# Kernel optimization log

Hardware: AMD Instinct MI355X
Metric: run time of the kernel (lower is better)

The kernel has to match this reference:

```python
import jax, jax.numpy as jnp
import numpy as np

FREQ_NUM = 3
MAX_STEP = 4
PERIODS = np.array([24.0, 7.0, 365.0], dtype=np.float32)  # ceil(sups - infs)
INFS = np.array([0.0, 0.0, 0.0], dtype=np.float32)
BS, H, W, L, D = 128, 56, 56, 64, 128
Z_DIM = 3 * H * W + L * D + D            # 17728
EMB_DIM = 2 * FREQ_NUM                   # sin/cos per frequency
IN_DIM = Z_DIM + 2 * EMB_DIM             # 17740
HID = 4096
N_POI, N_USER = 5000, 1000


def setup_inputs() -> dict:
    key = jax.random.key(0)
    ks = jax.random.split(key, 10)
    sups = jnp.asarray(PERIODS)
    return {
        "input_freq": jax.random.uniform(ks[0], (BS, H, W), jnp.float32),
        "input_seq": jax.random.randint(ks[1], (BS, L), 0, N_POI),
        "uid": jax.random.randint(ks[2], (BS,), 0, N_USER),
        "cur_time": jax.random.uniform(ks[3], (BS, FREQ_NUM), jnp.float32) * sups,
        "tar_time": jax.random.uniform(ks[4], (BS, FREQ_NUM), jnp.float32) * sups,
        "fuse_embed": jax.random.normal(ks[5], (N_POI + N_USER, D), jnp.float32),
        "W1": jax.random.normal(ks[6], (IN_DIM, HID), jnp.float32) / np.sqrt(IN_DIM),
        "b1": jnp.zeros((HID,), jnp.float32),
        "W2": jax.random.normal(ks[7], (HID, Z_DIM), jnp.float32) / np.sqrt(HID),
        "b2": jnp.zeros((Z_DIM,), jnp.float32),
        "n_poi": N_POI,
    }


def _time_grid(cur_time, tar_time):
    # Per-sample linspace with periodic wraparound; snapshot t0_ after each
    # micro-step assignment (intended semantics of the torch loop).
    periods = jnp.asarray(PERIODS)
    frac = jnp.linspace(0.0, 1.0, MAX_STEP)  # [4]
    rows = []
    t_cur = cur_time
    for j in range(FREQ_NUM):
        s = cur_time[:, j]
        e = tar_time[:, j]
        wrap = s > e
        e_adj = jnp.where(wrap, e + periods[j], e)
        inter = s[:, None] + (e_adj - s)[:, None] * frac[None, :]  # [bs,4]
        inter = jnp.where(wrap[:, None], jnp.mod(inter, periods[j]), inter)
        for k in range(MAX_STEP):
            t_cur = t_cur.at[:, j].set(inter[:, k])
            rows.append(t_cur)
    return jnp.stack(rows, axis=0)  # [4*freq_num, bs, freq_num]


def _time_embedding(T):
    # sinusoidal embedding per frequency band
    phase = 2.0 * jnp.pi * (T - jnp.asarray(INFS)) / jnp.asarray(PERIODS)
    return jnp.concatenate([jnp.sin(phase), jnp.cos(phase)], axis=-1)  # [S,bs,2F]


def reference(input_freq, input_seq, uid, cur_time, tar_time, fuse_embed,
              W1, b1, W2, b2, n_poi):
    bs = input_freq.shape[0]
    A = jnp.tile(input_freq[:, None], (1, 3, 1, 1)).reshape(bs, -1)     # [bs,3HW]
    x = fuse_embed[input_seq].transpose(0, 2, 1).reshape(bs, -1)        # [bs,D*L]
    u = fuse_embed[n_poi + uid].reshape(bs, -1)                          # [bs,D]
    z0 = jnp.concatenate([A, x, u], axis=-1)                             # [bs,Z_DIM]

    T = _time_grid(cur_time, tar_time)
    emb = _time_embedding(T)                                             # [S,bs,2F]

    def step(z, te):
        t0e, t1e = te
        inp = jnp.concatenate([z, t0e, t1e], axis=-1)
        dz = jnp.tanh(inp @ W1 + b1) @ W2 + b2
        return z + dz, None

    z, _ = jax.lax.scan(step, z0, (emb[:-1], emb[1:]))
    return z
```

## Files before the change

kernel.cpp:

```cpp
#include <hip/hip_runtime.h>
#include <math.h>

typedef __bf16 bf16;
typedef __bf16 bf16x8 __attribute__((ext_vector_type(8)));
typedef float f32x4 __attribute__((ext_vector_type(4)));

#define ZDIM 17728
#define HIDN 4096
#define BSZ 128
#define KC1 24
#define KC2 4

__device__ __forceinline__ void gl_lds16(const bf16* g, bf16* l) {
  __builtin_amdgcn_global_load_lds(
      (const __attribute__((address_space(1))) unsigned int*)g,
      (__attribute__((address_space(3))) unsigned int*)l, 16, 0, 0);
}

__global__ void k_cast_transpose(const float* __restrict__ src, bf16* __restrict__ dst,
                                 int K, int N) {
  __shared__ float t[64][33];
  int tx = threadIdx.x, ty = threadIdx.y;
  int n0 = blockIdx.x * 32, k0 = blockIdx.y * 64;
#pragma unroll
  for (int i = 0; i < 64; i += 8)
    t[ty + i][tx] = src[(size_t)(k0 + ty + i) * N + (n0 + tx)];
  __syncthreads();
#pragma unroll
  for (int i = 0; i < 32; i += 8) {
    int nl = ty + i;
    union { bf16 h[2]; unsigned u; } p;
    p.h[0] = (bf16)t[2 * tx][nl];
    p.h[1] = (bf16)t[2 * tx + 1][nl];
    *(unsigned*)&dst[(size_t)(n0 + nl) * K + k0 + 2 * tx] = p.u;
  }
}

__global__ void k_build_z0(const float* __restrict__ input_freq, const int* __restrict__ seq,
                           const int* __restrict__ uid, const float* __restrict__ fuse,
                           const int* __restrict__ n_poi_p,
                           float* __restrict__ z, bf16* __restrict__ zb) {
  int n = blockIdx.x * 256 + threadIdx.x;
  int b = blockIdx.y;
  if (n >= ZDIM) return;
  float v;
  if (n < 9408) {
    v = input_freq[b * 3136 + (n % 3136)];
  } else if (n < 17600) {
    int m = n - 9408;
    int d = m >> 6, l = m & 63;
    v = fuse[(size_t)seq[b * 64 + l] * 128 + d];
  } else {
    int d = n - 17600;
    v = fuse[(size_t)(n_poi_p[0] + uid[b]) * 128 + d];
  }
  size_t idx = (size_t)b * ZDIM + n;
  z[idx] = v;
  zb[idx] = (bf16)v;
}

__global__ void k_build_emb(const float* __restrict__ cur, const float* __restrict__ tar,
                            float* __restrict__ E) {
  int b = threadIdx.x;
  const float P[3] = {24.0f, 7.0f, 365.0f};
  const float TWO_PI = 6.283185307179586f;
  float t[3];
  for (int c = 0; c < 3; ++c) t[c] = cur[b * 3 + c];
  int r = 0;
  for (int j = 0; j < 3; ++j) {
    float s = cur[b * 3 + j], e = tar[b * 3 + j];
    bool wrap = s > e;
    float ea = wrap ? (e + P[j]) : e;
    for (int k = 0; k < 4; ++k) {
      float frac = (float)k / 3.0f;
      float v = s + (ea - s) * frac;
      if (wrap) v = v - floorf(v / P[j]) * P[j];
      t[j] = v;
      for (int c = 0; c < 3; ++c) {
        float ph = TWO_PI * t[c] / P[c];
        E[(r * BSZ + b) * 6 + c] = sinf(ph);
        E[(r * BSZ + b) * 6 + 3 + c] = cosf(ph);
      }
      ++r;
    }
  }
}

__global__ __launch_bounds__(256, 3) void k_gemm1(const bf16* __restrict__ A,
                                                  const bf16* __restrict__ Bt,
                                                  float* __restrict__ P) {
  __shared__ __align__(16) bf16 As[128 * 32];
  __shared__ __align__(16) bf16 Bs[128 * 32];
  const int tid = threadIdx.x;
  const int w = tid >> 6, lane = tid & 63;
  const int q = lane >> 4, r = lane & 15;
  const int nt = blockIdx.x, kc = blockIdx.y;
  const int nsteps = 23 + (kc < 2 ? 1 : 0);
  const int kstart = kc * 23 + (kc < 2 ? kc : 2);

  const int srow = lane >> 2, sslot = lane & 3;
  const int sg = sslot ^ ((srow >> 2) & 3);
  const int rA0 = (2 * w) * 16 + srow;
  const int rA1 = (2 * w + 1) * 16 + srow;
  long k0 = (long)kstart * 32;
  const bf16* pA0 = A + (size_t)rA0 * ZDIM + k0 + sg * 8;
  const bf16* pA1 = A + (size_t)rA1 * ZDIM + k0 + sg * 8;
  const bf16* pB0 = Bt + (size_t)(nt * 128 + rA0) * ZDIM + k0 + sg * 8;
  const bf16* pB1 = Bt + (size_t)(nt * 128 + rA1) * ZDIM + k0 + sg * 8;
  bf16* lA0 = &As[(2 * w) * 512];
  bf16* lA1 = &As[(2 * w + 1) * 512];
  bf16* lB0 = &Bs[(2 * w) * 512];
  bf16* lB1 = &Bs[(2 * w + 1) * 512];

  const int swr = (r >> 2) & 3;
  const int aoff = r * 32 + (q ^ swr) * 8;
  const int boff0 = (32 * w + r) * 32 + (q ^ swr) * 8;
  const int boff1 = boff0 + 512;

  f32x4 zero4 = {0.f, 0.f, 0.f, 0.f};
  f32x4 acc[8][2];
#pragma unroll
  for (int mb = 0; mb < 8; ++mb) { acc[mb][0] = zero4; acc[mb][1] = zero4; }

  for (int s = 0; s < nsteps; ++s) {
    gl_lds16(pA0, lA0); gl_lds16(pA1, lA1);
    gl_lds16(pB0, lB0); gl_lds16(pB1, lB1);
    pA0 += 32; pA1 += 32; pB0 += 32; pB1 += 32;
    __syncthreads();
    bf16x8 bfr0 = *(const bf16x8*)&Bs[boff0];
    bf16x8 bfr1 = *(const bf16x8*)&Bs[boff1];
#pragma unroll
    for (int mb = 0; mb < 8; ++mb) {
      bf16x8 afr = *(const bf16x8*)&As[mb * 512 + aoff];
      acc[mb][0] = __builtin_amdgcn_mfma_f32_16x16x32_bf16(afr, bfr0, acc[mb][0], 0, 0, 0);
      acc[mb][1] = __builtin_amdgcn_mfma_f32_16x16x32_bf16(afr, bfr1, acc[mb][1], 0, 0, 0);
    }
    __syncthreads();
  }

  float* Pk = P + (size_t)kc * (BSZ * HIDN);
#pragma unroll
  for (int i = 0; i < 2; ++i) {
    int n = nt * 128 + (2 * w + i) * 16 + r;
#pragma unroll
    for (int mb = 0; mb < 8; ++mb) {
#pragma unroll
      for (int reg = 0; reg < 4; ++reg) {
        int brow = mb * 16 + q * 4 + reg;
        Pk[(size_t)brow * HIDN + n] = acc[mb][i][reg];
      }
    }
  }
}

__global__ void k_epi1(const float* __restrict__ P, const float* __restrict__ b1,
                       const float* __restrict__ W1, const float* __restrict__ E,
                       int step, bf16* __restrict__ Hb) {
  int idx = blockIdx.x * 256 + threadIdx.x;
  int b = idx >> 12, n = idx & 4095;
  float s = b1[n];
#pragma unroll
  for (int c = 0; c < KC1; ++c) s += P[((size_t)c * BSZ + b) * HIDN + n];
  const float* e0 = E + ((size_t)step * BSZ + b) * 6;
  const float* e1 = e0 + BSZ * 6;
#pragma unroll
  for (int j = 0; j < 6; ++j) {
    s += e0[j] * W1[(size_t)(ZDIM + j) * HIDN + n];
    s += e1[j] * W1[(size_t)(ZDIM + 6 + j) * HIDN + n];
  }
  Hb[idx] = (bf16)tanhf(s);
}

__global__ __launch_bounds__(256, 4) void k_gemm2(const bf16* __restrict__ A,
                                                  const bf16* __restrict__ Bt,
                                                  float* __restrict__ P2) {
  __shared__ __align__(16) bf16 As[128 * 32];
  __shared__ __align__(16) bf16 Bs[64 * 32];
  const int tid = threadIdx.x;
  const int w = tid >> 6, lane = tid & 63;
  const int q = lane >> 4, r = lane & 15;
  const int nt = blockIdx.x;
  const int kc = blockIdx.y;
  const long k0 = (long)kc * 32 * 32;

  const int srow = lane >> 2, sslot = lane & 3;
  const int sg = sslot ^ ((srow >> 2) & 3);
  const int rA0 = (2 * w) * 16 + srow;
  const int rA1 = (2 * w + 1) * 16 + srow;
  const int rB = w * 16 + srow;
  const bf16* pA0 = A + (size_t)rA0 * HIDN + k0 + sg * 8;
  const bf16* pA1 = A + (size_t)rA1 * HIDN + k0 + sg * 8;
  const bf16* pB = Bt + (size_t)(nt * 64 + rB) * HIDN + k0 + sg * 8;
  bf16* lA0 = &As[(2 * w) * 512];
  bf16* lA1 = &As[(2 * w + 1) * 512];
  bf16* lB = &Bs[w * 512];

  const int swr = (r >> 2) & 3;
  const int aoff = r * 32 + (q ^ swr) * 8;
  const int boff = (w * 16 + r) * 32 + (q ^ swr) * 8;

  f32x4 zero4 = {0.f, 0.f, 0.f, 0.f};
  f32x4 acc[8];
#pragma unroll
  for (int mb = 0; mb < 8; ++mb) acc[mb] = zero4;

  for (int s = 0; s < 32; ++s) {
    gl_lds16(pA0, lA0); gl_lds16(pA1, lA1); gl_lds16(pB, lB);
    pA0 += 32; pA1 += 32; pB += 32;
    __syncthreads();
    bf16x8 bfr = *(const bf16x8*)&Bs[boff];
#pragma unroll
    for (int mb = 0; mb < 8; ++mb) {
      bf16x8 afr = *(const bf16x8*)&As[mb * 512 + aoff];
      acc[mb] = __builtin_amdgcn_mfma_f32_16x16x32_bf16(afr, bfr, acc[mb], 0, 0, 0);
    }
    __syncthreads();
  }

  float* Pk = P2 + (size_t)kc * (BSZ * ZDIM);
  int n = nt * 64 + w * 16 + r;
#pragma unroll
  for (int mb = 0; mb < 8; ++mb) {
#pragma unroll
    for (int reg = 0; reg < 4; ++reg) {
      int brow = mb * 16 + q * 4 + reg;
      Pk[(size_t)brow * ZDIM + n] = acc[mb][reg];
    }
  }
}

__global__ void k_epi2(const float* __restrict__ P2, const float* __restrict__ b2,
                       float* __restrict__ z, bf16* __restrict__ zb) {
  int idx = blockIdx.x * 256 + threadIdx.x;
  int n = idx % ZDIM;
  float s = b2[n];
#pragma unroll
  for (int c = 0; c < KC2; ++c) s += P2[(size_t)c * (BSZ * ZDIM) + idx];
  float v = z[idx] + s;
  z[idx] = v;
  zb[idx] = (bf16)v;
}

extern "C" void kernel_launch(void* const* d_in, const int* in_sizes, int n_in,
                              void* d_out, int out_size, void* d_ws, size_t ws_size,
                              hipStream_t stream) {
  const float* input_freq = (const float*)d_in[0];
  const int* seq = (const int*)d_in[1];
  const int* uid = (const int*)d_in[2];
  const float* cur = (const float*)d_in[3];
  const float* tar = (const float*)d_in[4];
  const float* fuse = (const float*)d_in[5];
  const float* W1 = (const float*)d_in[6];
  const float* b1 = (const float*)d_in[7];
  const float* W2 = (const float*)d_in[8];
  const float* b2 = (const float*)d_in[9];
  const int* n_poi = (const int*)d_in[10];
  float* z = (float*)d_out;

  char* ws = (char*)d_ws;
  bf16* W1t = (bf16*)ws;
  bf16* W2t = (bf16*)(ws + 145227776);
  bf16* Zb = (bf16*)(ws + 290455552);
  bf16* Hb = (bf16*)(ws + 294993920);
  float* P = (float*)(ws + 296042496);
  float* P2 = (float*)(ws + 296042496 + 50331648);
  float* E = (float*)(ws + 296042496 + 50331648 + 36306944);

  k_cast_transpose<<<dim3(HIDN / 32, ZDIM / 64), dim3(32, 8), 0, stream>>>(W1, W1t, ZDIM, HIDN);
  k_cast_transpose<<<dim3(ZDIM / 32, HIDN / 64), dim3(32, 8), 0, stream>>>(W2, W2t, HIDN, ZDIM);
  k_build_z0<<<dim3(70, BSZ), 256, 0, stream>>>(input_freq, seq, uid, fuse, n_poi, z, Zb);
  k_build_emb<<<1, BSZ, 0, stream>>>(cur, tar, E);

  for (int s = 0; s < 11; ++s) {
    k_gemm1<<<dim3(32, KC1), 256, 0, stream>>>(Zb, W1t, P);
    k_epi1<<<2048, 256, 0, stream>>>(P, b1, W1, E, s, Hb);
    k_gemm2<<<dim3(277, KC2), 256, 0, stream>>>(Hb, W2t, P2);
    k_epi2<<<8864, 256, 0, stream>>>(P2, b2, z, Zb);
  }
}
```

Measured before the change: 2.141 ms.

## Replace LDS-staged GEMMs with unified register-direct MFMA kernel and coalesce z0 gather

```diff
diff --git a/kernel.cpp b/kernel.cpp
--- a/kernel.cpp
+++ b/kernel.cpp
@@ -8,14 +8,8 @@
 #define ZDIM 17728
 #define HIDN 4096
 #define BSZ 128
-#define KC1 24
+#define KC1 16
 #define KC2 4
-
-__device__ __forceinline__ void gl_lds16(const bf16* g, bf16* l) {
-  __builtin_amdgcn_global_load_lds(
-      (const __attribute__((address_space(1))) unsigned int*)g,
-      (__attribute__((address_space(3))) unsigned int*)l, 16, 0, 0);
-}
 
 __global__ void k_cast_transpose(const float* __restrict__ src, bf16* __restrict__ dst,
                                  int K, int N) {
@@ -40,23 +34,32 @@
                            const int* __restrict__ uid, const float* __restrict__ fuse,
                            const int* __restrict__ n_poi_p,
                            float* __restrict__ z, bf16* __restrict__ zb) {
-  int n = blockIdx.x * 256 + threadIdx.x;
-  int b = blockIdx.y;
-  if (n >= ZDIM) return;
-  float v;
-  if (n < 9408) {
-    v = input_freq[b * 3136 + (n % 3136)];
-  } else if (n < 17600) {
-    int m = n - 9408;
+  __shared__ float X[64 * 129];
+  int b = blockIdx.x, tid = threadIdx.x;
+  float* zr = z + (size_t)b * ZDIM;
+  bf16* zbr = zb + (size_t)b * ZDIM;
+  for (int n = tid; n < 9408; n += 256) {
+    float v = input_freq[b * 3136 + (n % 3136)];
+    zr[n] = v; zbr[n] = (bf16)v;
+  }
+  {
+    int l = tid >> 2, c0 = (tid & 3) * 32;
+    const float* srcr = fuse + (size_t)seq[b * 64 + l] * 128 + c0;
+    float* dstr = X + l * 129 + c0;
+#pragma unroll
+    for (int i = 0; i < 32; i += 4)
+      *(f32x4*)&dstr[i] = *(const f32x4*)&srcr[i];
+  }
+  __syncthreads();
+  for (int m = tid; m < 8192; m += 256) {
     int d = m >> 6, l = m & 63;
-    v = fuse[(size_t)seq[b * 64 + l] * 128 + d];
-  } else {
-    int d = n - 17600;
-    v = fuse[(size_t)(n_poi_p[0] + uid[b]) * 128 + d];
-  }
-  size_t idx = (size_t)b * ZDIM + n;
-  z[idx] = v;
-  zb[idx] = (bf16)v;
+    float v = X[l * 129 + d];
+    zr[9408 + m] = v; zbr[9408 + m] = (bf16)v;
+  }
+  if (tid < 128) {
+    float v = fuse[(size_t)(n_poi_p[0] + uid[b]) * 128 + tid];
+    zr[17600 + tid] = v; zbr[17600 + tid] = (bf16)v;
+  }
 }
 
 __global__ void k_build_emb(const float* __restrict__ cur, const float* __restrict__ tar,
@@ -86,69 +89,47 @@
   }
 }
 
-__global__ __launch_bounds__(256, 3) void k_gemm1(const bf16* __restrict__ A,
-                                                  const bf16* __restrict__ Bt,
-                                                  float* __restrict__ P) {
-  __shared__ __align__(16) bf16 As[128 * 32];
-  __shared__ __align__(16) bf16 Bs[128 * 32];
+__global__ __launch_bounds__(256, 4) void k_gemm_rr(const bf16* __restrict__ A,
+                                                    const bf16* __restrict__ Bt,
+                                                    float* __restrict__ P,
+                                                    int Kdim, int Nout,
+                                                    int base, int rem) {
   const int tid = threadIdx.x;
   const int w = tid >> 6, lane = tid & 63;
   const int q = lane >> 4, r = lane & 15;
   const int nt = blockIdx.x, kc = blockIdx.y;
-  const int nsteps = 23 + (kc < 2 ? 1 : 0);
-  const int kstart = kc * 23 + (kc < 2 ? kc : 2);
-
-  const int srow = lane >> 2, sslot = lane & 3;
-  const int sg = sslot ^ ((srow >> 2) & 3);
-  const int rA0 = (2 * w) * 16 + srow;
-  const int rA1 = (2 * w + 1) * 16 + srow;
-  long k0 = (long)kstart * 32;
-  const bf16* pA0 = A + (size_t)rA0 * ZDIM + k0 + sg * 8;
-  const bf16* pA1 = A + (size_t)rA1 * ZDIM + k0 + sg * 8;
-  const bf16* pB0 = Bt + (size_t)(nt * 128 + rA0) * ZDIM + k0 + sg * 8;
-  const bf16* pB1 = Bt + (size_t)(nt * 128 + rA1) * ZDIM + k0 + sg * 8;
-  bf16* lA0 = &As[(2 * w) * 512];
-  bf16* lA1 = &As[(2 * w + 1) * 512];
-  bf16* lB0 = &Bs[(2 * w) * 512];
-  bf16* lB1 = &Bs[(2 * w + 1) * 512];
-
-  const int swr = (r >> 2) & 3;
-  const int aoff = r * 32 + (q ^ swr) * 8;
-  const int boff0 = (32 * w + r) * 32 + (q ^ swr) * 8;
-  const int boff1 = boff0 + 512;
-
-  f32x4 zero4 = {0.f, 0.f, 0.f, 0.f};
-  f32x4 acc[8][2];
-#pragma unroll
-  for (int mb = 0; mb < 8; ++mb) { acc[mb][0] = zero4; acc[mb][1] = zero4; }
-
+  const int nsteps = base + (kc < rem ? 1 : 0);
+  const long kstart = ((long)kc * base + (kc < rem ? kc : rem)) * 32;
+
+  const int n0 = nt * 64 + w * 16 + r;
+  const bf16* pB = Bt + (size_t)n0 * Kdim + kstart + q * 8;
+  const bf16* pA[8];
+#pragma unroll
+  for (int mb = 0; mb < 8; ++mb)
+    pA[mb] = A + (size_t)(mb * 16 + r) * Kdim + kstart + q * 8;
+
+  f32x4 acc[8] = {};
+#pragma unroll 2
   for (int s = 0; s < nsteps; ++s) {
-    gl_lds16(pA0, lA0); gl_lds16(pA1, lA1);
-    gl_lds16(pB0, lB0); gl_lds16(pB1, lB1);
-    pA0 += 32; pA1 += 32; pB0 += 32; pB1 += 32;
-    __syncthreads();
-    bf16x8 bfr0 = *(const bf16x8*)&Bs[boff0];
-    bf16x8 bfr1 = *(const bf16x8*)&Bs[boff1];
-#pragma unroll
-    for (int mb = 0; mb < 8; ++mb) {
-      bf16x8 afr = *(const bf16x8*)&As[mb * 512 + aoff];
-      acc[mb][0] = __builtin_amdgcn_mfma_f32_16x16x32_bf16(afr, bfr0, acc[mb][0], 0, 0, 0);
-      acc[mb][1] = __builtin_amdgcn_mfma_f32_16x16x32_bf16(afr, bfr1, acc[mb][1], 0, 0, 0);
-    }
-    __syncthreads();
-  }
-
-  float* Pk = P + (size_t)kc * (BSZ * HIDN);
-#pragma unroll
-  for (int i = 0; i < 2; ++i) {
-    int n = nt * 128 + (2 * w + i) * 16 + r;
-#pragma unroll
-    for (int mb = 0; mb < 8; ++mb) {
-#pragma unroll
-      for (int reg = 0; reg < 4; ++reg) {
-        int brow = mb * 16 + q * 4 + reg;
-        Pk[(size_t)brow * HIDN + n] = acc[mb][i][reg];
-      }
+    bf16x8 bfr = *(const bf16x8*)pB;
+    bf16x8 af[8];
+#pragma unroll
+    for (int mb = 0; mb < 8; ++mb) af[mb] = *(const bf16x8*)pA[mb];
+#pragma unroll
+    for (int mb = 0; mb < 8; ++mb)
+      acc[mb] = __builtin_amdgcn_mfma_f32_16x16x32_bf16(af[mb], bfr, acc[mb], 0, 0, 0);
+    pB += 32;
+#pragma unroll
+    for (int mb = 0; mb < 8; ++mb) pA[mb] += 32;
+  }
+
+  float* Pk = P + (size_t)kc * (BSZ * (size_t)Nout);
+#pragma unroll
+  for (int mb = 0; mb < 8; ++mb) {
+#pragma unroll
+    for (int reg = 0; reg < 4; ++reg) {
+      int m = mb * 16 + q * 4 + reg;
+      Pk[(size_t)m * Nout + n0] = acc[mb][reg];
     }
   }
 }
@@ -169,64 +150,6 @@
     s += e1[j] * W1[(size_t)(ZDIM + 6 + j) * HIDN + n];
   }
   Hb[idx] = (bf16)tanhf(s);
-}
-
-__global__ __launch_bounds__(256, 4) void k_gemm2(const bf16* __restrict__ A,
-                                                  const bf16* __restrict__ Bt,
-                                                  float* __restrict__ P2) {
-  __shared__ __align__(16) bf16 As[128 * 32];
-  __shared__ __align__(16) bf16 Bs[64 * 32];
-  const int tid = threadIdx.x;
-  const int w = tid >> 6, lane = tid & 63;
-  const int q = lane >> 4, r = lane & 15;
-  const int nt = blockIdx.x;
-  const int kc = blockIdx.y;
-  const long k0 = (long)kc * 32 * 32;
-
-  const int srow = lane >> 2, sslot = lane & 3;
-  const int sg = sslot ^ ((srow >> 2) & 3);
-  const int rA0 = (2 * w) * 16 + srow;
-  const int rA1 = (2 * w + 1) * 16 + srow;
-  const int rB = w * 16 + srow;
-  const bf16* pA0 = A + (size_t)rA0 * HIDN + k0 + sg * 8;
-  const bf16* pA1 = A + (size_t)rA1 * HIDN + k0 + sg * 8;
-  const bf16* pB = Bt + (size_t)(nt * 64 + rB) * HIDN + k0 + sg * 8;
-  bf16* lA0 = &As[(2 * w) * 512];
-  bf16* lA1 = &As[(2 * w + 1) * 512];
-  bf16* lB = &Bs[w * 512];
-
-  const int swr = (r >> 2) & 3;
-  const int aoff = r * 32 + (q ^ swr) * 8;
-  const int boff = (w * 16 + r) * 32 + (q ^ swr) * 8;
-
-  f32x4 zero4 = {0.f, 0.f, 0.f, 0.f};
-  f32x4 acc[8];
-#pragma unroll
-  for (int mb = 0; mb < 8; ++mb) acc[mb] = zero4;
-
-  for (int s = 0; s < 32; ++s) {
-    gl_lds16(pA0, lA0); gl_lds16(pA1, lA1); gl_lds16(pB, lB);
-    pA0 += 32; pA1 += 32; pB += 32;
-    __syncthreads();
-    bf16x8 bfr = *(const bf16x8*)&Bs[boff];
-#pragma unroll
-    for (int mb = 0; mb < 8; ++mb) {
-      bf16x8 afr = *(const bf16x8*)&As[mb * 512 + aoff];
-      acc[mb] = __builtin_amdgcn_mfma_f32_16x16x32_bf16(afr, bfr, acc[mb], 0, 0, 0);
-    }
-    __syncthreads();
-  }
-
-  float* Pk = P2 + (size_t)kc * (BSZ * ZDIM);
-  int n = nt * 64 + w * 16 + r;
-#pragma unroll
-  for (int mb = 0; mb < 8; ++mb) {
-#pragma unroll
-    for (int reg = 0; reg < 4; ++reg) {
-      int brow = mb * 16 + q * 4 + reg;
-      Pk[(size_t)brow * ZDIM + n] = acc[mb][reg];
-    }
-  }
 }
 
 __global__ void k_epi2(const float* __restrict__ P2, const float* __restrict__ b2,
@@ -263,18 +186,18 @@
   bf16* Zb = (bf16*)(ws + 290455552);
   bf16* Hb = (bf16*)(ws + 294993920);
   float* P = (float*)(ws + 296042496);
-  float* P2 = (float*)(ws + 296042496 + 50331648);
-  float* E = (float*)(ws + 296042496 + 50331648 + 36306944);
+  float* P2 = (float*)(ws + 296042496 + 33554432);
+  float* E = (float*)(ws + 296042496 + 33554432 + 36306944);
 
   k_cast_transpose<<<dim3(HIDN / 32, ZDIM / 64), dim3(32, 8), 0, stream>>>(W1, W1t, ZDIM, HIDN);
   k_cast_transpose<<<dim3(ZDIM / 32, HIDN / 64), dim3(32, 8), 0, stream>>>(W2, W2t, HIDN, ZDIM);
-  k_build_z0<<<dim3(70, BSZ), 256, 0, stream>>>(input_freq, seq, uid, fuse, n_poi, z, Zb);
+  k_build_z0<<<BSZ, 256, 0, stream>>>(input_freq, seq, uid, fuse, n_poi, z, Zb);
   k_build_emb<<<1, BSZ, 0, stream>>>(cur, tar, E);
 
   for (int s = 0; s < 11; ++s) {
-    k_gemm1<<<dim3(32, KC1), 256, 0, stream>>>(Zb, W1t, P);
+    k_gemm_rr<<<dim3(HIDN / 64, KC1), 256, 0, stream>>>(Zb, W1t, P, ZDIM, HIDN, 34, 10);
     k_epi1<<<2048, 256, 0, stream>>>(P, b1, W1, E, s, Hb);
-    k_gemm2<<<dim3(277, KC2), 256, 0, stream>>>(Hb, W2t, P2);
+    k_gemm_rr<<<dim3(ZDIM / 64, KC2), 256, 0, stream>>>(Hb, W2t, P2, HIDN, ZDIM, 32, 0);
     k_epi2<<<8864, 256, 0, stream>>>(P2, b2, z, Zb);
   }
 }
```

Result: slower. 4.287 ms (+100.3%).
